# Kernel tuning notes

Hardware: AMD Instinct MI355X
Metric: run time of the kernel (lower is better)

The kernel has to match this reference:

```python
import jax, jax.numpy as jnp
import numpy as np

EPS = 1e-6
NH, NKV, HD = 16, 8, 256
WIN = 1024
NE, TOPK = 32, 4
H, I = 2816, 704


def _rmsnorm(x, w, eps=EPS):
    x32 = x.astype(jnp.float32)
    n = x32 * jax.lax.rsqrt(jnp.mean(x32 * x32, axis=-1, keepdims=True) + eps)
    return n.astype(x.dtype) * w


def _rotate_half(x):
    x1, x2 = jnp.split(x, 2, axis=-1)
    return jnp.concatenate([-x2, x1], axis=-1)


def setup_inputs() -> dict:
    B, S = 1, 512
    key = jax.random.key(0)
    ks = jax.random.split(key, 10)
    sc = 0.02
    hidden_states = jax.random.normal(ks[0], (B, S, H), jnp.float32)
    # rope tables (sliding_attention: theta=10000, full rotary over head_dim)
    pos = np.arange(S, dtype=np.float64)
    inv = 1.0 / (10000.0 ** (np.arange(0, HD, 2, dtype=np.float64) / HD))
    fr = pos[:, None] * inv[None, :]
    emb = np.concatenate([fr, fr], axis=-1)
    cos = jnp.asarray(np.cos(emb)[None], jnp.float32)
    sin = jnp.asarray(np.sin(emb)[None], jnp.float32)
    return dict(
        hidden_states=hidden_states, cos=cos, sin=sin,
        ln_in_w=jnp.ones((H,), jnp.float32),
        ln_post_attn_w=jnp.ones((H,), jnp.float32),
        ln_pre_ffn_w=jnp.ones((H,), jnp.float32),
        ln_post_ffn_w=jnp.ones((H,), jnp.float32),
        q_w=jax.random.normal(ks[1], (NH * HD, H), jnp.float32) * sc,
        k_w=jax.random.normal(ks[2], (NKV * HD, H), jnp.float32) * sc,
        v_w=jax.random.normal(ks[3], (NKV * HD, H), jnp.float32) * sc,
        o_w=jax.random.normal(ks[4], (H, NH * HD), jnp.float32) * sc,
        q_norm_w=jnp.ones((HD,), jnp.float32),
        k_norm_w=jnp.ones((HD,), jnp.float32),
        router_w=jax.random.normal(ks[5], (NE, H), jnp.float32) * sc,
        router_scale=jnp.ones((H,), jnp.float32),
        w_gate=jax.random.normal(ks[6], (NE, I, H), jnp.float32) * sc,
        w_up=jax.random.normal(ks[7], (NE, I, H), jnp.float32) * sc,
        w_down=jax.random.normal(ks[8], (NE, H, I), jnp.float32) * sc,
    )


def reference(hidden_states, cos, sin, ln_in_w, ln_post_attn_w, ln_pre_ffn_w,
              ln_post_ffn_w, q_w, k_w, v_w, o_w, q_norm_w, k_norm_w,
              router_w, router_scale, w_gate, w_up, w_down):
    B, S, _ = hidden_states.shape
    # ---- attention block ----
    res = hidden_states
    h = _rmsnorm(hidden_states, ln_in_w)
    q = (h @ q_w.T).reshape(B, S, NH, HD)
    k = (h @ k_w.T).reshape(B, S, NKV, HD)
    v = (h @ v_w.T).reshape(B, S, NKV, HD)
    q = _rmsnorm(q, q_norm_w)
    k = _rmsnorm(k, k_norm_w)
    v = _rmsnorm(v, jnp.float32(1.0))  # v_norm has no scale
    c, s = cos[:, :, None, :], sin[:, :, None, :]
    q = q * c + _rotate_half(q) * s
    k = k * c + _rotate_half(k) * s
    kr = jnp.repeat(k, NH // NKV, axis=2)  # GQA expand
    vr = jnp.repeat(v, NH // NKV, axis=2)
    scores = jnp.einsum('bqnd,bknd->bnqk', q, kr)  # softmax scale = 1.0
    ii = jnp.arange(S)[:, None]
    jj = jnp.arange(S)[None, :]
    mask = (jj <= ii) & ((ii - jj) < WIN)  # causal + sliding window
    scores = jnp.where(mask, scores, jnp.finfo(scores.dtype).min)
    attn = jax.nn.softmax(scores, axis=-1)
    o = jnp.einsum('bnqk,bknd->bqnd', attn, vr).reshape(B, S, NH * HD)
    h = _rmsnorm(o @ o_w.T, ln_post_attn_w)
    x = res + h
    # ---- MoE block ----
    res = x
    h = _rmsnorm(x, ln_pre_ffn_w)
    t = h.reshape(B * S, H)
    # router: RMSNorm(no scale) * hidden^-0.5 * scale -> linear -> softmax -> topk
    t32 = t.astype(jnp.float32)
    n = (t32 * jax.lax.rsqrt(jnp.mean(t32 * t32, -1, keepdims=True) + EPS)).astype(t.dtype)
    n = n * (H ** -0.5) * router_scale
    probs = jax.nn.softmax(n @ router_w.T, axis=-1)
    topw, topi = jax.lax.top_k(probs, TOPK)
    topw = topw / jnp.sum(topw, axis=-1, keepdims=True)
    T = t.shape[0]
    combine = jnp.zeros((T, NE), t.dtype).at[jnp.arange(T)[:, None], topi].add(topw)
    # gated MLP per expert (dense eval + sparse combine == torch_moe math)
    g = jnp.einsum('th,eih->eti', t, w_gate)
    u = jnp.einsum('th,eih->eti', t, w_up)
    a = jax.nn.gelu(g, approximate=True) * u
    y = jnp.einsum('eti,ehi->eth', a, w_down)  # [E,T,H]
    moe = jnp.einsum('te,eth->th', combine, y).reshape(B, S, H)
    moe = _rmsnorm(moe, ln_post_ffn_w)
    return res + moe
```

## Files before the change

### kernel.cpp

```cpp
#include <hip/hip_runtime.h>

static constexpr int T_S   = 512;
static constexpr int H_DIM = 2816;
static constexpr int HD_   = 256;
static constexpr int N_E   = 32;
static constexpr int TOPK_ = 4;
static constexpr int I_DIM = 704;
static constexpr int Q_N   = 4096;
static constexpr int KV_N  = 2048;
static constexpr int QKV_N = 8192;
static constexpr float EPS_ = 1e-6f;

typedef __attribute__((ext_vector_type(4))) float f32x4;
typedef __attribute__((ext_vector_type(8))) short bf16x8;

static __device__ __forceinline__ ushort f2bf(float f) {
  uint u = __float_as_uint(f);
  u += 0x7fffu + ((u >> 16) & 1u);
  return (ushort)(u >> 16);
}
static __device__ __forceinline__ float bf2f(ushort u) {
  return __uint_as_float((uint)u << 16);
}
static __device__ __forceinline__ void split2(float x, ushort& h, ushort& l2) {
  h = f2bf(x);
  l2 = f2bf(x - bf2f(h));
}
static __device__ __forceinline__ void split8(const float4& a, const float4& b,
                                              uint4& H, uint4& L) {
  ushort h0,l0,h1,l1,h2,l2,h3,l3,h4,l4,h5,l5,h6,l6,h7,l7;
  split2(a.x,h0,l0); split2(a.y,h1,l1); split2(a.z,h2,l2); split2(a.w,h3,l3);
  split2(b.x,h4,l4); split2(b.y,h5,l5); split2(b.z,h6,l6); split2(b.w,h7,l7);
  H = (uint4){ (uint)h0|((uint)h1<<16), (uint)h2|((uint)h3<<16),
               (uint)h4|((uint)h5<<16), (uint)h6|((uint)h7<<16) };
  L = (uint4){ (uint)l0|((uint)l1<<16), (uint)l2|((uint)l3<<16),
               (uint)l4|((uint)l5<<16), (uint)l6|((uint)l7<<16) };
}
static __device__ __forceinline__ uint4 pack8(const float4& a, const float4& b) {
  return (uint4){ (uint)f2bf(a.x)|((uint)f2bf(a.y)<<16), (uint)f2bf(a.z)|((uint)f2bf(a.w)<<16),
                  (uint)f2bf(b.x)|((uint)f2bf(b.y)<<16), (uint)f2bf(b.z)|((uint)f2bf(b.w)<<16) };
}

static __device__ __forceinline__ float wave_sum(float v) {
  #pragma unroll
  for (int off = 1; off < 64; off <<= 1) v += __shfl_xor(v, off);
  return v;
}
static __device__ __forceinline__ float block_sum256(float v, float* sm) {
  v = wave_sum(v);
  int w = threadIdx.x >> 6, l = threadIdx.x & 63;
  if (l == 0) sm[w] = v;
  __syncthreads();
  float r = sm[0] + sm[1] + sm[2] + sm[3];
  __syncthreads();
  return r;
}

__global__ __launch_bounds__(256) void k_ln_in(
    const float* __restrict__ hid, const float* __restrict__ w,
    ushort* __restrict__ hhi, ushort* __restrict__ hlo) {
  __shared__ float sm[4];
  int t = blockIdx.x, tid = threadIdx.x;
  const float* row = hid + (size_t)t * H_DIM;
  float x[11]; float s = 0.f;
  #pragma unroll
  for (int j = 0; j < 11; ++j) { x[j] = row[tid + j*256]; s += x[j]*x[j]; }
  s = block_sum256(s, sm);
  float r = rsqrtf(s / (float)H_DIM + EPS_);
  #pragma unroll
  for (int j = 0; j < 11; ++j) {
    int idx = tid + j*256;
    float val = x[j]*r*w[idx];
    ushort h, l2; split2(val, h, l2);
    hhi[(size_t)t*H_DIM + idx] = h;
    hlo[(size_t)t*H_DIM + idx] = l2;
  }
}

__global__ __launch_bounds__(256, 2) void k_gemm_qkv(
    const ushort* __restrict__ Ah, const ushort* __restrict__ Al,
    const float* __restrict__ qw, const float* __restrict__ kw,
    const float* __restrict__ vw, float* __restrict__ Cp) {
  const int K = H_DIM, KS = H_DIM/2, NSs = KS/32;
  __shared__ ushort Ash[4][129][8], Asl[4][129][8];
  __shared__ ushort Bsh[4][65][8],  Bsl[4][65][8];
  int tid = threadIdx.x, w = tid >> 6, l = tid & 63;
  int n0 = blockIdx.x * 64, m0 = blockIdx.y * 128, kz = blockIdx.z;
  int kbase = kz * KS;
  const float* Bp = (n0 < Q_N) ? qw + (size_t)n0*K
                  : (n0 < Q_N+KV_N) ? kw + (size_t)(n0-Q_N)*K
                  : vw + (size_t)(n0-Q_N-KV_N)*K;
  float* C = Cp + (size_t)kz * T_S * QKV_N;
  const int l15 = l & 15, lq = l >> 4;
  const int wm = w >> 1, wn = w & 1;
  const int sar = tid >> 2, sak = tid & 3;
  const ushort* aph = Ah + (size_t)(m0 + sar)*K + kbase + sak*8;
  const ushort* apl = Al + (size_t)(m0 + sar)*K + kbase + sak*8;
  const float*  bp  = Bp + (size_t)sar*K + kbase + sak*8;
  uint4 arh0 = *(const uint4*)(aph);
  uint4 arh1 = *(const uint4*)(aph + (size_t)64*K);
  uint4 arl0 = *(const uint4*)(apl);
  uint4 arl1 = *(const uint4*)(apl + (size_t)64*K);
  float4 brA = *(const float4*)(bp), brB = *(const float4*)(bp + 4);
  f32x4 acc[4][2];
  #pragma unroll
  for (int a = 0; a < 4; ++a)
    #pragma unroll
    for (int b = 0; b < 2; ++b) acc[a][b] = (f32x4){0.f,0.f,0.f,0.f};
  for (int t = 0; t < NSs; ++t) {
    *(uint4*)&Ash[sak][sar][0]    = arh0;
    *(uint4*)&Ash[sak][64+sar][0] = arh1;
    *(uint4*)&Asl[sak][sar][0]    = arl0;
    *(uint4*)&Asl[sak][64+sar][0] = arl1;
    { uint4 H, L; split8(brA, brB, H, L);
      *(uint4*)&Bsh[sak][sar][0] = H;
      *(uint4*)&Bsl[sak][sar][0] = L; }
    __syncthreads();
    if (t + 1 < NSs) {
      int k0 = (t+1)*32;
      arh0 = *(const uint4*)(aph + k0);
      arh1 = *(const uint4*)(aph + (size_t)64*K + k0);
      arl0 = *(const uint4*)(apl + k0);
      arl1 = *(const uint4*)(apl + (size_t)64*K + k0);
      brA = *(const float4*)(bp + k0); brB = *(const float4*)(bp + k0 + 4);
    }
    bf16x8 bh[2], bl[2];
    #pragma unroll
    for (int nf = 0; nf < 2; ++nf) {
      bh[nf] = *(bf16x8*)&Bsh[lq][wn*32 + nf*16 + l15][0];
      bl[nf] = *(bf16x8*)&Bsl[lq][wn*32 + nf*16 + l15][0];
    }
    #pragma unroll
    for (int mf = 0; mf < 4; ++mf) {
      bf16x8 ah = *(bf16x8*)&Ash[lq][wm*64 + mf*16 + l15][0];
      bf16x8 al = *(bf16x8*)&Asl[lq][wm*64 + mf*16 + l15][0];
      #pragma unroll
      for (int nf = 0; nf < 2; ++nf) {
        acc[mf][nf] = __builtin_amdgcn_mfma_f32_16x16x32_bf16(ah, bh[nf], acc[mf][nf], 0, 0, 0);
        acc[mf][nf] = __builtin_amdgcn_mfma_f32_16x16x32_bf16(ah, bl[nf], acc[mf][nf], 0, 0, 0);
        acc[mf][nf] = __builtin_amdgcn_mfma_f32_16x16x32_bf16(al, bh[nf], acc[mf][nf], 0, 0, 0);
      }
    }
    __syncthreads();
  }
  #pragma unroll
  for (int mf = 0; mf < 4; ++mf)
    #pragma unroll
    for (int nf = 0; nf < 2; ++nf)
      #pragma unroll
      for (int r = 0; r < 4; ++r)
        C[(size_t)(m0 + wm*64 + mf*16 + lq*4 + r)*QKV_N + n0 + wn*32 + nf*16 + l15] = acc[mf][nf][r];
}

__global__ __launch_bounds__(64) void k_norm_rope(
    const float* __restrict__ qkvf0, const float* __restrict__ qkvf1,
    const float* __restrict__ cosb, const float* __restrict__ sinb,
    const float* __restrict__ qnw, const float* __restrict__ knw,
    ushort* __restrict__ qh, ushort* __restrict__ ql,
    ushort* __restrict__ vth, ushort* __restrict__ vtl) {
  int bid = blockIdx.x;
  int token = bid >> 5, ch = bid & 31;
  int l = threadIdx.x;
  int col; const float* wp = nullptr; bool rope = true; int vch = -1;
// ... 196 lines not shown
  const ushort* apl = Al + (size_t)(m0 + sar)*K + kbase + sak*8;
  const float*  bp  = ow + (size_t)(n0 + sar)*K + kbase + sak*8;
  uint4 arh0 = *(const uint4*)(aph);
  uint4 arh1 = *(const uint4*)(aph + (size_t)64*K);
  uint4 arl0 = *(const uint4*)(apl);
  uint4 arl1 = *(const uint4*)(apl + (size_t)64*K);
  float4 brA = *(const float4*)(bp), brB = *(const float4*)(bp + 4);
  f32x4 acc[4][2];
  #pragma unroll
  for (int a = 0; a < 4; ++a)
    #pragma unroll
    for (int b = 0; b < 2; ++b) acc[a][b] = (f32x4){0.f,0.f,0.f,0.f};
  for (int t = 0; t < NSs; ++t) {
    *(uint4*)&Ash[sak][sar][0]    = arh0;
    *(uint4*)&Ash[sak][64+sar][0] = arh1;
    *(uint4*)&Asl[sak][sar][0]    = arl0;
    *(uint4*)&Asl[sak][64+sar][0] = arl1;
    { uint4 H, L; split8(brA, brB, H, L);
      *(uint4*)&Bsh[sak][sar][0] = H;
      *(uint4*)&Bsl[sak][sar][0] = L; }
    __syncthreads();
    if (t + 1 < NSs) {
      int k0 = (t+1)*32;
      arh0 = *(const uint4*)(aph + k0);
      arh1 = *(const uint4*)(aph + (size_t)64*K + k0);
      arl0 = *(const uint4*)(apl + k0);
      arl1 = *(const uint4*)(apl + (size_t)64*K + k0);
      brA = *(const float4*)(bp + k0); brB = *(const float4*)(bp + k0 + 4);
    }
    bf16x8 bh[2], bl[2];
    #pragma unroll
    for (int nf = 0; nf < 2; ++nf) {
      bh[nf] = *(bf16x8*)&Bsh[lq][wn*32 + nf*16 + l15][0];
      bl[nf] = *(bf16x8*)&Bsl[lq][wn*32 + nf*16 + l15][0];
    }
    #pragma unroll
    for (int mf = 0; mf < 4; ++mf) {
      bf16x8 ah = *(bf16x8*)&Ash[lq][wm*64 + mf*16 + l15][0];
      bf16x8 al = *(bf16x8*)&Asl[lq][wm*64 + mf*16 + l15][0];
      #pragma unroll
      for (int nf = 0; nf < 2; ++nf) {
        acc[mf][nf] = __builtin_amdgcn_mfma_f32_16x16x32_bf16(ah, bh[nf], acc[mf][nf], 0, 0, 0);
        acc[mf][nf] = __builtin_amdgcn_mfma_f32_16x16x32_bf16(ah, bl[nf], acc[mf][nf], 0, 0, 0);
        acc[mf][nf] = __builtin_amdgcn_mfma_f32_16x16x32_bf16(al, bh[nf], acc[mf][nf], 0, 0, 0);
      }
    }
    __syncthreads();
  }
  #pragma unroll
  for (int mf = 0; mf < 4; ++mf)
    #pragma unroll
    for (int nf = 0; nf < 2; ++nf)
      #pragma unroll
      for (int r = 0; r < 4; ++r)
        C[(size_t)(m0 + wm*64 + mf*16 + lq*4 + r)*H_DIM + n0 + wn*32 + nf*16 + l15] = acc[mf][nf][r];
}

__global__ void k_zero_counts(int* counts) {
  if (threadIdx.x < N_E) counts[threadIdx.x] = 0;
}

__global__ __launch_bounds__(256) void k_fuse_router(
    const float* __restrict__ hid, const float* __restrict__ aproj0,
    const float* __restrict__ aproj1,
    const float* __restrict__ w_pa, const float* __restrict__ w_pf,
    const float* __restrict__ rscale, const float* __restrict__ rw,
    float* __restrict__ xout, ushort* __restrict__ tbf,
    float* __restrict__ topw, int* __restrict__ counts, int* __restrict__ lists) {
  __shared__ float sm[4];
  __shared__ float nrow[H_DIM];
  __shared__ float lg[N_E];
  int t = blockIdx.x, tid = threadIdx.x;
  float ap[11], hd[11]; float s = 0.f;
  #pragma unroll
  for (int j = 0; j < 11; ++j) {
    int idx = tid + j*256;
    ap[j] = aproj0[(size_t)t*H_DIM + idx] + aproj1[(size_t)t*H_DIM + idx];
    hd[j] = hid[(size_t)t*H_DIM + idx];
    s += ap[j]*ap[j];
  }
  s = block_sum256(s, sm);
  float r1 = rsqrtf(s / (float)H_DIM + EPS_);
  float x[11]; float s2 = 0.f;
  #pragma unroll
  for (int j = 0; j < 11; ++j) {
    int idx = tid + j*256;
    x[j] = hd[j] + ap[j]*r1*w_pa[idx];
    s2 += x[j]*x[j];
    xout[(size_t)t*H_DIM + idx] = x[j];
  }
  s2 = block_sum256(s2, sm);
  float r2 = rsqrtf(s2 / (float)H_DIM + EPS_);
  float tv[11]; float s3 = 0.f;
  #pragma unroll
  for (int j = 0; j < 11; ++j) {
    int idx = tid + j*256;
    tv[j] = x[j]*r2*w_pf[idx];
    s3 += tv[j]*tv[j];
    tbf[(size_t)t*H_DIM + idx] = f2bf(tv[j]);
  }
  s3 = block_sum256(s3, sm);
  float r3 = rsqrtf(s3 / (float)H_DIM + EPS_) * rsqrtf((float)H_DIM);
  #pragma unroll
  for (int j = 0; j < 11; ++j) {
    int idx = tid + j*256;
    nrow[idx] = tv[j]*r3*rscale[idx];
  }
  __syncthreads();
  int w = tid >> 6, l = tid & 63;
  #pragma unroll
  for (int ei = 0; ei < 8; ++ei) {
    int e = w*8 + ei;
    const float* rwp = rw + (size_t)e*H_DIM;
    float p = 0.f;
    #pragma unroll 4
    for (int j = 0; j < 44; ++j) p += nrow[l + j*64] * rwp[l + j*64];
    p = wave_sum(p);
    if (l == 0) lg[e] = p;
  }
  __syncthreads();
  if (w == 0) {
    float le = (l < 32) ? lg[l] : -3e38f;
    float m = le;
    #pragma unroll
    for (int off = 1; off < 64; off <<= 1) m = fmaxf(m, __shfl_xor(m, off));
    float p = (l < 32) ? __expf(le - m) : -2.f;
    float v = p; int vi = (l < 32) ? l : 999;
    float selv[TOPK_]; int seli[TOPK_];
    for (int sx = 0; sx < TOPK_; ++sx) {
      float bv = v; int bi = vi;
      #pragma unroll
      for (int off = 1; off < 64; off <<= 1) {
        float ov = __shfl_xor(bv, off); int oi = __shfl_xor(bi, off);
        if (ov > bv || (ov == bv && oi < bi)) { bv = ov; bi = oi; }
      }
      selv[sx] = bv; seli[sx] = bi;
      if (vi == bi) v = -1.f;
    }
    if (l == 0) {
      float wsum = selv[0]+selv[1]+selv[2]+selv[3];
      for (int sx = 0; sx < TOPK_; ++sx) {
        topw[t*TOPK_ + sx] = selv[sx]/wsum;
        int e = seli[sx];
        int pos = atomicAdd(&counts[e], 1);
        lists[e*T_S + pos] = t*TOPK_ + sx;
      }
    }
  }
}

__global__ __launch_bounds__(256, 2) void k_moe_gateup(
    const ushort* __restrict__ tbf, const float* __restrict__ wg,
    const float* __restrict__ wu, const int* __restrict__ counts,
    const int* __restrict__ lists, ushort* __restrict__ abf) {
  const int K = H_DIM, NS = K/32;
  __shared__ ushort As[4][65][8];
  __shared__ ushort Bg[4][129][8], Bu[4][129][8];
  __shared__ int lls[64];
  int tid = threadIdx.x, w = tid >> 6, l = tid & 63;
  int e = blockIdx.y, n0 = blockIdx.x * 128, m0 = blockIdx.z * 64;
  int ne = counts[e];
  if (m0 >= ne) return;
  const int* list = lists + e*T_S;
  if (tid < 64) lls[tid] = (m0 + tid < ne) ? list[m0 + tid] : list[0];
  __syncthreads();
  const int l15 = l & 15, lq = l >> 4;
  const int sar = tid >> 2, sak = tid & 3;
  int tok = lls[sar] >> 2;
  const ushort* ap = tbf + (size_t)tok*K + sak*8;
  int ng0 = n0 + sar, ng1 = n0 + 64 + sar;
  ng0 = (ng0 < I_DIM) ? ng0 : I_DIM-1;
  ng1 = (ng1 < I_DIM) ? ng1 : I_DIM-1;
  const float* gp0 = wg + ((size_t)e*I_DIM + ng0)*K + sak*8;
  const float* gp1 = wg + ((size_t)e*I_DIM + ng1)*K + sak*8;
  const float* up0 = wu + ((size_t)e*I_DIM + ng0)*K + sak*8;
  const float* up1 = wu + ((size_t)e*I_DIM + ng1)*K + sak*8;
  uint4 ar; float4 g0a,g0b,g1a,g1b,u0a,u0b,u1a,u1b;
  ar  = *(const uint4*)(ap);
  g0a = *(const float4*)(gp0); g0b = *(const float4*)(gp0 + 4);
  g1a = *(const float4*)(gp1); g1b = *(const float4*)(gp1 + 4);
  u0a = *(const float4*)(up0); u0b = *(const float4*)(up0 + 4);
  u1a = *(const float4*)(up1); u1b = *(const float4*)(up1 + 4);
  f32x4 ag[4][2], au[4][2];
  #pragma unroll
  for (int a = 0; a < 4; ++a)
    #pragma unroll
    for (int b = 0; b < 2; ++b) { ag[a][b] = (f32x4){0.f,0.f,0.f,0.f}; au[a][b] = (f32x4){0.f,0.f,0.f,0.f}; }
  for (int t = 0; t < NS; ++t) {
    *(uint4*)&As[sak][sar][0] = ar;
    *(uint4*)&Bg[sak][sar][0]    = pack8(g0a, g0b);
    *(uint4*)&Bg[sak][64+sar][0] = pack8(g1a, g1b);
    *(uint4*)&Bu[sak][sar][0]    = pack8(u0a, u0b);
    *(uint4*)&Bu[sak][64+sar][0] = pack8(u1a, u1b);
    __syncthreads();
    if (t + 1 < NS) {
      int k0 = (t+1)*32;
      ar  = *(const uint4*)(ap + k0);
      g0a = *(const float4*)(gp0 + k0); g0b = *(const float4*)(gp0 + k0 + 4);
      g1a = *(const float4*)(gp1 + k0); g1b = *(const float4*)(gp1 + k0 + 4);
      u0a = *(const float4*)(up0 + k0); u0b = *(const float4*)(up0 + k0 + 4);
      u1a = *(const float4*)(up1 + k0); u1b = *(const float4*)(up1 + k0 + 4);
    }
    bf16x8 bg[2], bu[2];
    #pragma unroll
    for (int nf = 0; nf < 2; ++nf) {
      bg[nf] = *(bf16x8*)&Bg[lq][w*32 + nf*16 + l15][0];
      bu[nf] = *(bf16x8*)&Bu[lq][w*32 + nf*16 + l15][0];
    }
    #pragma unroll
    for (int mf = 0; mf < 4; ++mf) {
      bf16x8 af = *(bf16x8*)&As[lq][mf*16 + l15][0];
      #pragma unroll
      for (int nf = 0; nf < 2; ++nf) {
        ag[mf][nf] = __builtin_amdgcn_mfma_f32_16x16x32_bf16(af, bg[nf], ag[mf][nf], 0, 0, 0);
        au[mf][nf] = __builtin_amdgcn_mfma_f32_16x16x32_bf16(af, bu[nf], au[mf][nf], 0, 0, 0);
      }
    }
    __syncthreads();
  }
  #pragma unroll
  for (int mf = 0; mf < 4; ++mf) {
    #pragma unroll
    for (int r = 0; r < 4; ++r) {
      int row = mf*16 + lq*4 + r;
      if (m0 + row < ne) {
        #pragma unroll
        for (int nf = 0; nf < 2; ++nf) {
          int col = n0 + w*32 + nf*16 + l15;
          if (col < I_DIM) {
            float g = ag[mf][nf][r], u = au[mf][nf][r];
            float th = tanhf(0.7978845608f*(g + 0.044715f*g*g*g));
            float a = 0.5f*g*(1.f + th)*u;
            abf[((size_t)e*T_S + m0 + row)*I_DIM + col] = f2bf(a);
          }
        }
      }
    }
  }
}

__global__ __launch_bounds__(256, 2) void k_moe_down(
    const ushort* __restrict__ abf, const float* __restrict__ wd,
    const int* __restrict__ counts, const int* __restrict__ lists,
    float* __restrict__ yall) {
  const int K = I_DIM, NS = K/32;
  __shared__ ushort As[4][65][8];
  __shared__ ushort Bs[4][129][8];
  __shared__ int lls[64];
  int tid = threadIdx.x, w = tid >> 6, l = tid & 63;
  int e = blockIdx.y, n0 = blockIdx.x * 128, m0 = blockIdx.z * 64;
  int ne = counts[e];
  if (m0 >= ne) return;
  const int* list = lists + e*T_S;
  if (tid < 64) lls[tid] = (m0 + tid < ne) ? list[m0 + tid] : 0;
  __syncthreads();
  const int l15 = l & 15, lq = l >> 4;
  const int sar = tid >> 2, sak = tid & 3;
  const ushort* ap = abf + ((size_t)e*T_S + m0 + sar)*K + sak*8;
  const float* bp0 = wd + ((size_t)e*H_DIM + n0 + sar)*K + sak*8;
  const float* bp1 = wd + ((size_t)e*H_DIM + n0 + 64 + sar)*K + sak*8;
  uint4 ar; float4 b0a,b0b,b1a,b1b;
  ar  = *(const uint4*)(ap);
  b0a = *(const float4*)(bp0); b0b = *(const float4*)(bp0 + 4);
  b1a = *(const float4*)(bp1); b1b = *(const float4*)(bp1 + 4);
  f32x4 acc[4][2];
  #pragma unroll
  for (int a = 0; a < 4; ++a)
    #pragma unroll
    for (int b = 0; b < 2; ++b) acc[a][b] = (f32x4){0.f,0.f,0.f,0.f};
  for (int t = 0; t < NS; ++t) {
    *(uint4*)&As[sak][sar][0] = ar;
    *(uint4*)&Bs[sak][sar][0]    = pack8(b0a, b0b);
    *(uint4*)&Bs[sak][64+sar][0] = pack8(b1a, b1b);
    __syncthreads();
    if (t + 1 < NS) {
      int k0 = (t+1)*32;
      ar  = *(const uint4*)(ap + k0);
      b0a = *(const float4*)(bp0 + k0); b0b = *(const float4*)(bp0 + k0 + 4);
      b1a = *(const float4*)(bp1 + k0); b1b = *(const float4*)(bp1 + k0 + 4);
    }
    bf16x8 bf[2];
    #pragma unroll
    for (int nf = 0; nf < 2; ++nf)
      bf[nf] = *(bf16x8*)&Bs[lq][w*32 + nf*16 + l15][0];
    #pragma unroll
    for (int mf = 0; mf < 4; ++mf) {
      bf16x8 af = *(bf16x8*)&As[lq][mf*16 + l15][0];
      #pragma unroll
      for (int nf = 0; nf < 2; ++nf)
        acc[mf][nf] = __builtin_amdgcn_mfma_f32_16x16x32_bf16(af, bf[nf], acc[mf][nf], 0, 0, 0);
    }
    __syncthreads();
  }
  #pragma unroll
  for (int mf = 0; mf < 4; ++mf)
    #pragma unroll
    for (int r = 0; r < 4; ++r) {
      int row = mf*16 + lq*4 + r;
      if (m0 + row < ne) {
        int en = lls[row];
        #pragma unroll
        for (int nf = 0; nf < 2; ++nf)
          yall[(size_t)en*H_DIM + n0 + w*32 + nf*16 + l15] = acc[mf][nf][r];
      }
    }
}

__global__ __launch_bounds__(256) void k_combine(
    const float* __restrict__ yall, const float* __restrict__ topw,
    const float* __restrict__ xin, const float* __restrict__ w_pff,
    float* __restrict__ out) {
  __shared__ float sm[4];
  int t = blockIdx.x, tid = threadIdx.x;
  float w0 = topw[t*4+0], w1 = topw[t*4+1], w2 = topw[t*4+2], w3 = topw[t*4+3];
  const float* y0 = yall + (size_t)(t*4+0)*H_DIM;
  const float* y1 = yall + (size_t)(t*4+1)*H_DIM;
  const float* y2 = yall + (size_t)(t*4+2)*H_DIM;
  const float* y3 = yall + (size_t)(t*4+3)*H_DIM;
  float m[11]; float s = 0.f;
  #pragma unroll
  for (int j = 0; j < 11; ++j) {
    int idx = tid + j*256;
    m[j] = w0*y0[idx] + w1*y1[idx] + w2*y2[idx] + w3*y3[idx];
    s += m[j]*m[j];
  }
  s = block_sum256(s, sm);
  float r = rsqrtf(s / (float)H_DIM + EPS_);
  #pragma unroll
  for (int j = 0; j < 11; ++j) {
    int idx = tid + j*256;
    out[(size_t)t*H_DIM + idx] = xin[(size_t)t*H_DIM + idx] + m[j]*r*w_pff[idx];
  }
}

extern "C" void kernel_launch(void* const* d_in, const int* in_sizes, int n_in,
                              void* d_out, int out_size, void* d_ws, size_t ws_size,
                              hipStream_t stream) {
  (void)in_sizes; (void)n_in; (void)out_size; (void)ws_size;
  const float* hid   = (const float*)d_in[0];
  const float* cosb  = (const float*)d_in[1];
  const float* sinb  = (const float*)d_in[2];
  const float* w_in  = (const float*)d_in[3];
  const float* w_pa  = (const float*)d_in[4];
  const float* w_pf  = (const float*)d_in[5];
  const float* w_pff = (const float*)d_in[6];
  const float* qw    = (const float*)d_in[7];
  const float* kw    = (const float*)d_in[8];
  const float* vw    = (const float*)d_in[9];
  const float* ow    = (const float*)d_in[10];
  const float* qnw   = (const float*)d_in[11];
  const float* knw   = (const float*)d_in[12];
  const float* rw    = (const float*)d_in[13];
  const float* rsc   = (const float*)d_in[14];
  const float* wg    = (const float*)d_in[15];
  const float* wu    = (const float*)d_in[16];
  const float* wd    = (const float*)d_in[17];

  char* ws = (char*)d_ws;
  size_t off = 0;
  auto alloc = [&](size_t sz) { size_t o = off; off += (sz + 255) & ~(size_t)255; return o; };
  size_t oR1  = alloc(33554432);
  size_t ohh  = alloc((size_t)T_S*H_DIM*2);
  size_t ohl  = alloc((size_t)T_S*H_DIM*2);
  size_t oqh  = alloc((size_t)T_S*QKV_N*2);
  size_t oql  = alloc((size_t)T_S*QKV_N*2);
  size_t ovh  = alloc((size_t)8*HD_*T_S*2);
  size_t ovl  = alloc((size_t)8*HD_*T_S*2);
  size_t ox   = alloc((size_t)T_S*H_DIM*4);
  size_t otbf = alloc((size_t)T_S*H_DIM*2);
  size_t otw  = alloc((size_t)T_S*TOPK_*4);
  size_t ocnt = alloc((size_t)N_E*4);
  size_t olst = alloc((size_t)N_E*T_S*4);

  const size_t APRJ_SLICE = (size_t)T_S * H_DIM * 4;

  float*  qkvf0 = (float*)(ws + oR1);
  float*  qkvf1 = (float*)(ws + oR1 + 16777216);
  ushort* o_hi  = (ushort*)(ws + oR1);
  ushort* o_lo  = (ushort*)(ws + oR1 + 4194304);
  float*  aprj0 = (float*)(ws + oR1 + 8388608);
  float*  aprj1 = (float*)(ws + oR1 + 8388608 + APRJ_SLICE);
  float*  yall  = (float*)(ws + oR1);
  ushort* abf   = (ushort*)(ws + ohh);

  k_ln_in<<<dim3(T_S), dim3(256), 0, stream>>>(hid, w_in, (ushort*)(ws+ohh), (ushort*)(ws+ohl));
  k_gemm_qkv<<<dim3(128, 4, 2), dim3(256), 0, stream>>>((ushort*)(ws+ohh), (ushort*)(ws+ohl),
                                                        qw, kw, vw, qkvf0);
  k_norm_rope<<<dim3(T_S*32), dim3(64), 0, stream>>>(qkvf0, qkvf1, cosb, sinb, qnw, knw,
                                                     (ushort*)(ws+oqh), (ushort*)(ws+oql),
                                                     (ushort*)(ws+ovh), (ushort*)(ws+ovl));
  k_attn<<<dim3(8, 16), dim3(256), 0, stream>>>((ushort*)(ws+oqh), (ushort*)(ws+oql),
                                                (ushort*)(ws+ovh), (ushort*)(ws+ovl), o_hi, o_lo);
  k_gemm_oproj<<<dim3(44, 4, 2), dim3(256), 0, stream>>>(o_hi, o_lo, ow, aprj0);
  k_zero_counts<<<dim3(1), dim3(64), 0, stream>>>((int*)(ws+ocnt));
  k_fuse_router<<<dim3(T_S), dim3(256), 0, stream>>>(hid, aprj0, aprj1, w_pa, w_pf, rsc, rw,
                                                     (float*)(ws+ox), (ushort*)(ws+otbf),
                                                     (float*)(ws+otw), (int*)(ws+ocnt), (int*)(ws+olst));
  k_moe_gateup<<<dim3(6, N_E, 8), dim3(256), 0, stream>>>((ushort*)(ws+otbf), wg, wu,
                                                          (int*)(ws+ocnt), (int*)(ws+olst), abf);
  k_moe_down<<<dim3(22, N_E, 8), dim3(256), 0, stream>>>(abf, wd,
                                                         (int*)(ws+ocnt), (int*)(ws+olst), yall);
  k_combine<<<dim3(T_S), dim3(256), 0, stream>>>(yall, (float*)(ws+otw), (float*)(ws+ox),
                                                 w_pff, (float*)d_out);
}
```

Measured before the change: 623.1 us.

## Retile MoE gate/up to narrow N tiles and deepen K step to 64

The gate/up expert GEMM tile shrinks from 128 to 32 output columns, so the grid grows from 6 to 22 column blocks per expert. With 704 = 22*32 the ragged-edge clamping goes away, and the four waves are arranged 2x2 over M and N. Both the gate/up and down kernels now stage 64 K-elements per iteration instead of 32, halving the number of barrier-separated steps and issuing wider per-thread global loads. The cost is that the token activations are reloaded by more blocks, with fewer MFMAs per wave per step and more LDS and registers in use.

Result: slower. 684.5 us (+9.9%).

```diff
diff --git a/kernel.cpp b/kernel.cpp
--- a/kernel.cpp
+++ b/kernel.cpp
@@ -512,99 +512,82 @@
     const ushort* __restrict__ tbf, const float* __restrict__ wg,
     const float* __restrict__ wu, const int* __restrict__ counts,
     const int* __restrict__ lists, ushort* __restrict__ abf) {
-  const int K = H_DIM, NS = K/32;
-  __shared__ ushort As[4][65][8];
-  __shared__ ushort Bg[4][129][8], Bu[4][129][8];
+  const int K = H_DIM, NS = K/64;
+  __shared__ ushort As[8][65][8];
+  __shared__ ushort Bg[8][33][8], Bu[8][33][8];
   __shared__ int lls[64];
   int tid = threadIdx.x, w = tid >> 6, l = tid & 63;
-  int e = blockIdx.y, n0 = blockIdx.x * 128, m0 = blockIdx.z * 64;
+  int e = blockIdx.y, n0 = blockIdx.x * 32, m0 = blockIdx.z * 64;
   int ne = counts[e];
   if (m0 >= ne) return;
   const int* list = lists + e*T_S;
   if (tid < 64) lls[tid] = (m0 + tid < ne) ? list[m0 + tid] : list[0];
   __syncthreads();
   const int l15 = l & 15, lq = l >> 4;
-  const int sar = tid >> 2, sak = tid & 3;
-  int tok = lls[sar] >> 2;
-  const ushort* ap = tbf + (size_t)tok*K + sak*8;
-  int ng0 = n0 + sar, ng1 = n0 + 64 + sar;
-  ng0 = (ng0 < I_DIM) ? ng0 : I_DIM-1;
-  ng1 = (ng1 < I_DIM) ? ng1 : I_DIM-1;
-  const float* gp0 = wg + ((size_t)e*I_DIM + ng0)*K + sak*8;
-  const float* gp1 = wg + ((size_t)e*I_DIM + ng1)*K + sak*8;
-  const float* up0 = wu + ((size_t)e*I_DIM + ng0)*K + sak*8;
-  const float* up1 = wu + ((size_t)e*I_DIM + ng1)*K + sak*8;
-  uint4 ar; float4 g0a,g0b,g1a,g1b,u0a,u0b,u1a,u1b;
-  ar  = *(const uint4*)(ap);
-  g0a = *(const float4*)(gp0); g0b = *(const float4*)(gp0 + 4);
-  g1a = *(const float4*)(gp1); g1b = *(const float4*)(gp1 + 4);
-  u0a = *(const float4*)(up0); u0b = *(const float4*)(up0 + 4);
-  u1a = *(const float4*)(up1); u1b = *(const float4*)(up1 + 4);
-  f32x4 ag[4][2], au[4][2];
-  #pragma unroll
-  for (int a = 0; a < 4; ++a)
-    #pragma unroll
-    for (int b = 0; b < 2; ++b) { ag[a][b] = (f32x4){0.f,0.f,0.f,0.f}; au[a][b] = (f32x4){0.f,0.f,0.f,0.f}; }
+  const int arow = tid >> 2, aop = (tid & 3) * 2;
+  int tok = lls[arow] >> 2;
+  const ushort* ap = tbf + (size_t)tok*K + aop*8;
+  const int bhalf = tid >> 7, brow = (tid & 127) >> 2, bq = tid & 3;
+  const float* bptr = (bhalf ? wu : wg) + ((size_t)e*I_DIM + n0 + brow)*K + bq*16;
+  uint4 a0 = *(const uint4*)(ap), a1 = *(const uint4*)(ap + 8);
+  float4 b0 = *(const float4*)(bptr),      b1 = *(const float4*)(bptr + 4);
+  float4 b2 = *(const float4*)(bptr + 8),  b3 = *(const float4*)(bptr + 12);
+  const int wm = w >> 1, wn = w & 1;
+  f32x4 ag[2], au[2];
+  #pragma unroll
+  for (int i = 0; i < 2; ++i) { ag[i] = (f32x4){0.f,0.f,0.f,0.f}; au[i] = (f32x4){0.f,0.f,0.f,0.f}; }
   for (int t = 0; t < NS; ++t) {
-    *(uint4*)&As[sak][sar][0] = ar;
-    *(uint4*)&Bg[sak][sar][0]    = pack8(g0a, g0b);
-    *(uint4*)&Bg[sak][64+sar][0] = pack8(g1a, g1b);
-    *(uint4*)&Bu[sak][sar][0]    = pack8(u0a, u0b);
-    *(uint4*)&Bu[sak][64+sar][0] = pack8(u1a, u1b);
+    *(uint4*)&As[aop][arow][0]   = a0;
+    *(uint4*)&As[aop+1][arow][0] = a1;
+    if (bhalf == 0) {
+      *(uint4*)&Bg[bq*2][brow][0]   = pack8(b0, b1);
+      *(uint4*)&Bg[bq*2+1][brow][0] = pack8(b2, b3);
+    } else {
+      *(uint4*)&Bu[bq*2][brow][0]   = pack8(b0, b1);
+      *(uint4*)&Bu[bq*2+1][brow][0] = pack8(b2, b3);
+    }
     __syncthreads();
     if (t + 1 < NS) {
-      int k0 = (t+1)*32;
-      ar  = *(const uint4*)(ap + k0);
-      g0a = *(const float4*)(gp0 + k0); g0b = *(const float4*)(gp0 + k0 + 4);
-      g1a = *(const float4*)(gp1 + k0); g1b = *(const float4*)(gp1 + k0 + 4);
-      u0a = *(const float4*)(up0 + k0); u0b = *(const float4*)(up0 + k0 + 4);
-      u1a = *(const float4*)(up1 + k0); u1b = *(const float4*)(up1 + k0 + 4);
-    }
-    bf16x8 bg[2], bu[2];
-    #pragma unroll
-    for (int nf = 0; nf < 2; ++nf) {
-      bg[nf] = *(bf16x8*)&Bg[lq][w*32 + nf*16 + l15][0];
-      bu[nf] = *(bf16x8*)&Bu[lq][w*32 + nf*16 + l15][0];
-    }
-    #pragma unroll
-    for (int mf = 0; mf < 4; ++mf) {
-      bf16x8 af = *(bf16x8*)&As[lq][mf*16 + l15][0];
-      #pragma unroll
-      for (int nf = 0; nf < 2; ++nf) {
-        ag[mf][nf] = __builtin_amdgcn_mfma_f32_16x16x32_bf16(af, bg[nf], ag[mf][nf], 0, 0, 0);
-        au[mf][nf] = __builtin_amdgcn_mfma_f32_16x16x32_bf16(af, bu[nf], au[mf][nf], 0, 0, 0);
-      }
-    }
-    __syncthreads();
-  }
-  #pragma unroll
-  for (int mf = 0; mf < 4; ++mf) {
+      int k0 = (t+1)*64;
+      a0 = *(const uint4*)(ap + k0); a1 = *(const uint4*)(ap + k0 + 8);
+      b0 = *(const float4*)(bptr + k0);      b1 = *(const float4*)(bptr + k0 + 4);
+      b2 = *(const float4*)(bptr + k0 + 8);  b3 = *(const float4*)(bptr + k0 + 12);
+    }
+    #pragma unroll
+    for (int kc = 0; kc < 2; ++kc) {
+      int pl = kc*4 + lq;
+      bf16x8 bgf = *(bf16x8*)&Bg[pl][wn*16 + l15][0];
+      bf16x8 buf = *(bf16x8*)&Bu[pl][wn*16 + l15][0];
+      #pragma unroll
+      for (int mf = 0; mf < 2; ++mf) {
+        bf16x8 af = *(bf16x8*)&As[pl][wm*32 + mf*16 + l15][0];
+        ag[mf] = __builtin_amdgcn_mfma_f32_16x16x32_bf16(af, bgf, ag[mf], 0, 0, 0);
+        au[mf] = __builtin_amdgcn_mfma_f32_16x16x32_bf16(af, buf, au[mf], 0, 0, 0);
+      }
+    }
+    __syncthreads();
+  }
+  #pragma unroll
+  for (int mf = 0; mf < 2; ++mf)
     #pragma unroll
     for (int r = 0; r < 4; ++r) {
-      int row = mf*16 + lq*4 + r;
+      int row = wm*32 + mf*16 + lq*4 + r;
       if (m0 + row < ne) {
-        #pragma unroll
-        for (int nf = 0; nf < 2; ++nf) {
-          int col = n0 + w*32 + nf*16 + l15;
-          if (col < I_DIM) {
-            float g = ag[mf][nf][r], u = au[mf][nf][r];
-            float th = tanhf(0.7978845608f*(g + 0.044715f*g*g*g));
-            float a = 0.5f*g*(1.f + th)*u;
-            abf[((size_t)e*T_S + m0 + row)*I_DIM + col] = f2bf(a);
-          }
-        }
-      }
-    }
-  }
+        float g = ag[mf][r], u = au[mf][r];
+        float th = tanhf(0.7978845608f*(g + 0.044715f*g*g*g));
+        float a = 0.5f*g*(1.f + th)*u;
+        abf[((size_t)e*T_S + m0 + row)*I_DIM + n0 + wn*16 + l15] = f2bf(a);
+      }
+    }
 }
 
 __global__ __launch_bounds__(256, 2) void k_moe_down(
     const ushort* __restrict__ abf, const float* __restrict__ wd,
     const int* __restrict__ counts, const int* __restrict__ lists,
     float* __restrict__ yall) {
-  const int K = I_DIM, NS = K/32;
-  __shared__ ushort As[4][65][8];
-  __shared__ ushort Bs[4][129][8];
+  const int K = I_DIM, NS = K/64;
+  __shared__ ushort As[8][65][8];
+  __shared__ ushort Bs[8][129][8];
   __shared__ int lls[64];
   int tid = threadIdx.x, w = tid >> 6, l = tid & 63;
   int e = blockIdx.y, n0 = blockIdx.x * 128, m0 = blockIdx.z * 64;
@@ -614,40 +597,47 @@
   if (tid < 64) lls[tid] = (m0 + tid < ne) ? list[m0 + tid] : 0;
   __syncthreads();
   const int l15 = l & 15, lq = l >> 4;
-  const int sar = tid >> 2, sak = tid & 3;
-  const ushort* ap = abf + ((size_t)e*T_S + m0 + sar)*K + sak*8;
-  const float* bp0 = wd + ((size_t)e*H_DIM + n0 + sar)*K + sak*8;
-  const float* bp1 = wd + ((size_t)e*H_DIM + n0 + 64 + sar)*K + sak*8;
-  uint4 ar; float4 b0a,b0b,b1a,b1b;
-  ar  = *(const uint4*)(ap);
-  b0a = *(const float4*)(bp0); b0b = *(const float4*)(bp0 + 4);
-  b1a = *(const float4*)(bp1); b1b = *(const float4*)(bp1 + 4);
+  const int arow = tid >> 2, aop = (tid & 3) * 2;
+  const ushort* ap = abf + ((size_t)e*T_S + m0 + arow)*K + aop*8;
+  const int brow = tid >> 1, bo = (tid & 1) * 4;
+  const float* bp = wd + ((size_t)e*H_DIM + n0 + brow)*K + bo*8;
+  uint4 a0 = *(const uint4*)(ap), a1 = *(const uint4*)(ap + 8);
+  float4 c0 = *(const float4*)(bp),      c1 = *(const float4*)(bp + 4);
+  float4 c2 = *(const float4*)(bp + 8),  c3 = *(const float4*)(bp + 12);
+  float4 c4 = *(const float4*)(bp + 16), c5 = *(const float4*)(bp + 20);
+  float4 c6 = *(const float4*)(bp + 24), c7 = *(const float4*)(bp + 28);
   f32x4 acc[4][2];
   #pragma unroll
   for (int a = 0; a < 4; ++a)
     #pragma unroll
     for (int b = 0; b < 2; ++b) acc[a][b] = (f32x4){0.f,0.f,0.f,0.f};
   for (int t = 0; t < NS; ++t) {
-    *(uint4*)&As[sak][sar][0] = ar;
-    *(uint4*)&Bs[sak][sar][0]    = pack8(b0a, b0b);
-    *(uint4*)&Bs[sak][64+sar][0] = pack8(b1a, b1b);
+    *(uint4*)&As[aop][arow][0]   = a0;
+    *(uint4*)&As[aop+1][arow][0] = a1;
+    *(uint4*)&Bs[bo][brow][0]   = pack8(c0, c1);
+    *(uint4*)&Bs[bo+1][brow][0] = pack8(c2, c3);
+    *(uint4*)&Bs[bo+2][brow][0] = pack8(c4, c5);
+    *(uint4*)&Bs[bo+3][brow][0] = pack8(c6, c7);
     __syncthreads();
     if (t + 1 < NS) {
-      int k0 = (t+1)*32;
-      ar  = *(const uint4*)(ap + k0);
-      b0a = *(const float4*)(bp0 + k0); b0b = *(const float4*)(bp0 + k0 + 4);
-      b1a = *(const float4*)(bp1 + k0); b1b = *(const float4*)(bp1 + k0 + 4);
-    }
-    bf16x8 bf[2];
-    #pragma unroll
-    for (int nf = 0; nf < 2; ++nf)
-      bf[nf] = *(bf16x8*)&Bs[lq][w*32 + nf*16 + l15][0];
-    #pragma unroll
-    for (int mf = 0; mf < 4; ++mf) {
-      bf16x8 af = *(bf16x8*)&As[lq][mf*16 + l15][0];
-      #pragma unroll
-      for (int nf = 0; nf < 2; ++nf)
-        acc[mf][nf] = __builtin_amdgcn_mfma_f32_16x16x32_bf16(af, bf[nf], acc[mf][nf], 0, 0, 0);
+      int k0 = (t+1)*64;
+      a0 = *(const uint4*)(ap + k0); a1 = *(const uint4*)(ap + k0 + 8);
+      c0 = *(const float4*)(bp + k0);      c1 = *(const float4*)(bp + k0 + 4);
+      c2 = *(const float4*)(bp + k0 + 8);  c3 = *(const float4*)(bp + k0 + 12);
+      c4 = *(const float4*)(bp + k0 + 16); c5 = *(const float4*)(bp + k0 + 20);
+      c6 = *(const float4*)(bp + k0 + 24); c7 = *(const float4*)(bp + k0 + 28);
+    }
+    #pragma unroll
+    for (int kc = 0; kc < 2; ++kc) {
+      int pl = kc*4 + lq;
+      bf16x8 bf0 = *(bf16x8*)&Bs[pl][w*32 + l15][0];
+      bf16x8 bf1 = *(bf16x8*)&Bs[pl][w*32 + 16 + l15][0];
+      #pragma unroll
+      for (int mf = 0; mf < 4; ++mf) {
+        bf16x8 af = *(bf16x8*)&As[pl][mf*16 + l15][0];
+        acc[mf][0] = __builtin_amdgcn_mfma_f32_16x16x32_bf16(af, bf0, acc[mf][0], 0, 0, 0);
+        acc[mf][1] = __builtin_amdgcn_mfma_f32_16x16x32_bf16(af, bf1, acc[mf][1], 0, 0, 0);
+      }
     }
     __syncthreads();
   }
@@ -755,8 +745,8 @@
   k_fuse_router<<<dim3(T_S), dim3(256), 0, stream>>>(hid, aprj0, aprj1, w_pa, w_pf, rsc, rw,
                                                      (float*)(ws+ox), (ushort*)(ws+otbf),
                                                      (float*)(ws+otw), (int*)(ws+ocnt), (int*)(ws+olst));
-  k_moe_gateup<<<dim3(6, N_E, 8), dim3(256), 0, stream>>>((ushort*)(ws+otbf), wg, wu,
-                                                          (int*)(ws+ocnt), (int*)(ws+olst), abf);
+  k_moe_gateup<<<dim3(22, N_E, 8), dim3(256), 0, stream>>>((ushort*)(ws+otbf), wg, wu,
+                                                           (int*)(ws+ocnt), (int*)(ws+olst), abf);
   k_moe_down<<<dim3(22, N_E, 8), dim3(256), 0, stream>>>(abf, wd,
                                                          (int*)(ws+ocnt), (int*)(ws+olst), yall);
   k_combine<<<dim3(T_S), dim3(256), 0, stream>>>(yall, (float*)(ws+otw), (float*)(ws+ox),
```

## Split-K MoE GEMMs with 128-row tiles and separate GELU reduction pass

Applied to the files above, without the earlier changes.

The gate/up GEMM is split four ways along K with 128x64 tiles, writing fp32 partials indexed by slot. A new kernel sums the partials and applies GELU*up into bf16. The down GEMM is split two ways along K with 128x128 tiles, and the combine kernel adds the two partials. The aim is to fill the GPU better despite the uneven per-expert token counts and to reuse weight loads across more rows. The cost is extra fp32 partial traffic, a larger workspace and one more kernel launch.

New measurement: 610.9 us. No clear change (-1.9%).

```diff
diff --git a/kernel.cpp b/kernel.cpp
--- a/kernel.cpp
+++ b/kernel.cpp
@@ -9,6 +9,7 @@
 static constexpr int Q_N   = 4096;
 static constexpr int KV_N  = 2048;
 static constexpr int QKV_N = 8192;
+static constexpr int NSLOT = 2048;
 static constexpr float EPS_ = 1e-6f;
 
 typedef __attribute__((ext_vector_type(4))) float f32x4;
@@ -511,176 +512,200 @@
 __global__ __launch_bounds__(256, 2) void k_moe_gateup(
     const ushort* __restrict__ tbf, const float* __restrict__ wg,
     const float* __restrict__ wu, const int* __restrict__ counts,
-    const int* __restrict__ lists, ushort* __restrict__ abf) {
-  const int K = H_DIM, NS = K/32;
-  __shared__ ushort As[4][65][8];
-  __shared__ ushort Bg[4][129][8], Bu[4][129][8];
-  __shared__ int lls[64];
+    const int* __restrict__ lists, float* __restrict__ pg, float* __restrict__ pu) {
+  const int K = H_DIM, KS = K/4, NS = KS/32;
+  __shared__ ushort As[4][129][8];
+  __shared__ ushort Bg[4][65][8], Bu[4][65][8];
+  __shared__ int lls[128];
   int tid = threadIdx.x, w = tid >> 6, l = tid & 63;
-  int e = blockIdx.y, n0 = blockIdx.x * 128, m0 = blockIdx.z * 64;
+  int e = blockIdx.y, n0 = blockIdx.x * 64;
+  int mz = blockIdx.z >> 2, kz = blockIdx.z & 3;
+  int m0 = mz * 128, kbase = kz * KS;
   int ne = counts[e];
   if (m0 >= ne) return;
   const int* list = lists + e*T_S;
-  if (tid < 64) lls[tid] = (m0 + tid < ne) ? list[m0 + tid] : list[0];
+  if (tid < 128) lls[tid] = (m0 + tid < ne) ? list[m0 + tid] : list[0];
   __syncthreads();
   const int l15 = l & 15, lq = l >> 4;
-  const int sar = tid >> 2, sak = tid & 3;
-  int tok = lls[sar] >> 2;
-  const ushort* ap = tbf + (size_t)tok*K + sak*8;
-  int ng0 = n0 + sar, ng1 = n0 + 64 + sar;
-  ng0 = (ng0 < I_DIM) ? ng0 : I_DIM-1;
-  ng1 = (ng1 < I_DIM) ? ng1 : I_DIM-1;
-  const float* gp0 = wg + ((size_t)e*I_DIM + ng0)*K + sak*8;
-  const float* gp1 = wg + ((size_t)e*I_DIM + ng1)*K + sak*8;
-  const float* up0 = wu + ((size_t)e*I_DIM + ng0)*K + sak*8;
-  const float* up1 = wu + ((size_t)e*I_DIM + ng1)*K + sak*8;
-  uint4 ar; float4 g0a,g0b,g1a,g1b,u0a,u0b,u1a,u1b;
-  ar  = *(const uint4*)(ap);
-  g0a = *(const float4*)(gp0); g0b = *(const float4*)(gp0 + 4);
-  g1a = *(const float4*)(gp1); g1b = *(const float4*)(gp1 + 4);
-  u0a = *(const float4*)(up0); u0b = *(const float4*)(up0 + 4);
-  u1a = *(const float4*)(up1); u1b = *(const float4*)(up1 + 4);
+  const int wm = w >> 1, wn = w & 1;
+  const int arow = tid >> 1, aoct = (tid & 1) * 2;
+  const ushort* ap = tbf + (size_t)(lls[arow] >> 2)*K + kbase + aoct*8;
+  const int bhalf = tid >> 7, brow = (tid & 127) >> 1, boct = (tid & 1) * 2;
+  const float* bp = (bhalf ? wu : wg) + ((size_t)e*I_DIM + n0 + brow)*K + kbase + boct*8;
+  uint4 a0 = *(const uint4*)(ap), a1 = *(const uint4*)(ap + 8);
+  float4 b0 = *(const float4*)(bp),     b1 = *(const float4*)(bp + 4);
+  float4 b2 = *(const float4*)(bp + 8), b3 = *(const float4*)(bp + 12);
   f32x4 ag[4][2], au[4][2];
   #pragma unroll
   for (int a = 0; a < 4; ++a)
     #pragma unroll
     for (int b = 0; b < 2; ++b) { ag[a][b] = (f32x4){0.f,0.f,0.f,0.f}; au[a][b] = (f32x4){0.f,0.f,0.f,0.f}; }
   for (int t = 0; t < NS; ++t) {
-    *(uint4*)&As[sak][sar][0] = ar;
-    *(uint4*)&Bg[sak][sar][0]    = pack8(g0a, g0b);
-    *(uint4*)&Bg[sak][64+sar][0] = pack8(g1a, g1b);
-    *(uint4*)&Bu[sak][sar][0]    = pack8(u0a, u0b);
-    *(uint4*)&Bu[sak][64+sar][0] = pack8(u1a, u1b);
+    *(uint4*)&As[aoct][arow][0]   = a0;
+    *(uint4*)&As[aoct+1][arow][0] = a1;
+    if (bhalf == 0) {
+      *(uint4*)&Bg[boct][brow][0]   = pack8(b0, b1);
+      *(uint4*)&Bg[boct+1][brow][0] = pack8(b2, b3);
+    } else {
+      *(uint4*)&Bu[boct][brow][0]   = pack8(b0, b1);
+      *(uint4*)&Bu[boct+1][brow][0] = pack8(b2, b3);
+    }
     __syncthreads();
     if (t + 1 < NS) {
       int k0 = (t+1)*32;
-      ar  = *(const uint4*)(ap + k0);
-      g0a = *(const float4*)(gp0 + k0); g0b = *(const float4*)(gp0 + k0 + 4);
-      g1a = *(const float4*)(gp1 + k0); g1b = *(const float4*)(gp1 + k0 + 4);
-      u0a = *(const float4*)(up0 + k0); u0b = *(const float4*)(up0 + k0 + 4);
-      u1a = *(const float4*)(up1 + k0); u1b = *(const float4*)(up1 + k0 + 4);
-    }
-    bf16x8 bg[2], bu[2];
+      a0 = *(const uint4*)(ap + k0); a1 = *(const uint4*)(ap + k0 + 8);
+      b0 = *(const float4*)(bp + k0);     b1 = *(const float4*)(bp + k0 + 4);
+      b2 = *(const float4*)(bp + k0 + 8); b3 = *(const float4*)(bp + k0 + 12);
+    }
+    bf16x8 bgf[2], buf_[2];
     #pragma unroll
     for (int nf = 0; nf < 2; ++nf) {
-      bg[nf] = *(bf16x8*)&Bg[lq][w*32 + nf*16 + l15][0];
-      bu[nf] = *(bf16x8*)&Bu[lq][w*32 + nf*16 + l15][0];
+      bgf[nf]  = *(bf16x8*)&Bg[lq][wn*32 + nf*16 + l15][0];
+      buf_[nf] = *(bf16x8*)&Bu[lq][wn*32 + nf*16 + l15][0];
     }
     #pragma unroll
     for (int mf = 0; mf < 4; ++mf) {
-      bf16x8 af = *(bf16x8*)&As[lq][mf*16 + l15][0];
+      bf16x8 af = *(bf16x8*)&As[lq][wm*64 + mf*16 + l15][0];
       #pragma unroll
       for (int nf = 0; nf < 2; ++nf) {
-        ag[mf][nf] = __builtin_amdgcn_mfma_f32_16x16x32_bf16(af, bg[nf], ag[mf][nf], 0, 0, 0);
-        au[mf][nf] = __builtin_amdgcn_mfma_f32_16x16x32_bf16(af, bu[nf], au[mf][nf], 0, 0, 0);
-      }
-    }
-    __syncthreads();
-  }
-  #pragma unroll
-  for (int mf = 0; mf < 4; ++mf) {
+        ag[mf][nf] = __builtin_amdgcn_mfma_f32_16x16x32_bf16(af, bgf[nf],  ag[mf][nf], 0, 0, 0);
+        au[mf][nf] = __builtin_amdgcn_mfma_f32_16x16x32_bf16(af, buf_[nf], au[mf][nf], 0, 0, 0);
+      }
+    }
+    __syncthreads();
+  }
+  const size_t PSL = (size_t)NSLOT * I_DIM;
+  #pragma unroll
+  for (int mf = 0; mf < 4; ++mf)
     #pragma unroll
     for (int r = 0; r < 4; ++r) {
-      int row = mf*16 + lq*4 + r;
+      int row = wm*64 + mf*16 + lq*4 + r;
       if (m0 + row < ne) {
+        size_t base = (size_t)kz*PSL + (size_t)lls[row]*I_DIM + n0 + wn*32;
         #pragma unroll
         for (int nf = 0; nf < 2; ++nf) {
-          int col = n0 + w*32 + nf*16 + l15;
-          if (col < I_DIM) {
-            float g = ag[mf][nf][r], u = au[mf][nf][r];
-            float th = tanhf(0.7978845608f*(g + 0.044715f*g*g*g));
-            float a = 0.5f*g*(1.f + th)*u;
-            abf[((size_t)e*T_S + m0 + row)*I_DIM + col] = f2bf(a);
-          }
+          pg[base + nf*16 + l15] = ag[mf][nf][r];
+          pu[base + nf*16 + l15] = au[mf][nf][r];
         }
       }
     }
-  }
+}
+
+__global__ __launch_bounds__(192) void k_gelu_reduce(
+    const float* __restrict__ pg, const float* __restrict__ pu,
+    ushort* __restrict__ abf) {
+  int sidx = blockIdx.x, c = threadIdx.x;
+  if (c >= 176) return;
+  const size_t S4 = (size_t)NSLOT * I_DIM / 4;
+  const float4* g = (const float4*)(pg + (size_t)sidx*I_DIM) + c;
+  const float4* u = (const float4*)(pu + (size_t)sidx*I_DIM) + c;
+  float4 gs = g[0], us = u[0];
+  #pragma unroll
+  for (int k = 1; k < 4; ++k) {
+    float4 gk = g[k*S4], uk = u[k*S4];
+    gs.x += gk.x; gs.y += gk.y; gs.z += gk.z; gs.w += gk.w;
+    us.x += uk.x; us.y += uk.y; us.z += uk.z; us.w += uk.w;
+  }
+  float go[4] = {gs.x, gs.y, gs.z, gs.w}, uo[4] = {us.x, us.y, us.z, us.w};
+  ushort o[4];
+  #pragma unroll
+  for (int i = 0; i < 4; ++i) {
+    float gg = go[i];
+    float th = tanhf(0.7978845608f*(gg + 0.044715f*gg*gg*gg));
+    o[i] = f2bf(0.5f*gg*(1.f + th)*uo[i]);
+  }
+  *(ushort4*)(abf + (size_t)sidx*I_DIM + c*4) = *(ushort4*)o;
 }
 
 __global__ __launch_bounds__(256, 2) void k_moe_down(
     const ushort* __restrict__ abf, const float* __restrict__ wd,
     const int* __restrict__ counts, const int* __restrict__ lists,
-    float* __restrict__ yall) {
-  const int K = I_DIM, NS = K/32;
-  __shared__ ushort As[4][65][8];
+    float* __restrict__ yp) {
+  const int K = I_DIM, KS = K/2, NS = KS/32;
+  __shared__ ushort As[4][129][8];
   __shared__ ushort Bs[4][129][8];
-  __shared__ int lls[64];
+  __shared__ int lls[128];
   int tid = threadIdx.x, w = tid >> 6, l = tid & 63;
-  int e = blockIdx.y, n0 = blockIdx.x * 128, m0 = blockIdx.z * 64;
+  int e = blockIdx.y, n0 = blockIdx.x * 128;
+  int mz = blockIdx.z >> 1, kz = blockIdx.z & 1;
+  int m0 = mz * 128, kbase = kz * KS;
   int ne = counts[e];
   if (m0 >= ne) return;
   const int* list = lists + e*T_S;
-  if (tid < 64) lls[tid] = (m0 + tid < ne) ? list[m0 + tid] : 0;
+  if (tid < 128) lls[tid] = (m0 + tid < ne) ? list[m0 + tid] : 0;
   __syncthreads();
   const int l15 = l & 15, lq = l >> 4;
-  const int sar = tid >> 2, sak = tid & 3;
-  const ushort* ap = abf + ((size_t)e*T_S + m0 + sar)*K + sak*8;
-  const float* bp0 = wd + ((size_t)e*H_DIM + n0 + sar)*K + sak*8;
-  const float* bp1 = wd + ((size_t)e*H_DIM + n0 + 64 + sar)*K + sak*8;
-  uint4 ar; float4 b0a,b0b,b1a,b1b;
-  ar  = *(const uint4*)(ap);
-  b0a = *(const float4*)(bp0); b0b = *(const float4*)(bp0 + 4);
-  b1a = *(const float4*)(bp1); b1b = *(const float4*)(bp1 + 4);
-  f32x4 acc[4][2];
+  const int wm = w >> 1, wn = w & 1;
+  const int arow = tid >> 1, aoct = (tid & 1) * 2;
+  const ushort* ap = abf + (size_t)lls[arow]*K + kbase + aoct*8;
+  const int brow = tid >> 1, boct = (tid & 1) * 2;
+  const float* bp = wd + ((size_t)e*H_DIM + n0 + brow)*K + kbase + boct*8;
+  uint4 a0 = *(const uint4*)(ap), a1 = *(const uint4*)(ap + 8);
+  float4 b0 = *(const float4*)(bp),     b1 = *(const float4*)(bp + 4);
+  float4 b2 = *(const float4*)(bp + 8), b3 = *(const float4*)(bp + 12);
+  f32x4 acc[4][4];
   #pragma unroll
   for (int a = 0; a < 4; ++a)
     #pragma unroll
-    for (int b = 0; b < 2; ++b) acc[a][b] = (f32x4){0.f,0.f,0.f,0.f};
+    for (int b = 0; b < 4; ++b) acc[a][b] = (f32x4){0.f,0.f,0.f,0.f};
   for (int t = 0; t < NS; ++t) {
-    *(uint4*)&As[sak][sar][0] = ar;
-    *(uint4*)&Bs[sak][sar][0]    = pack8(b0a, b0b);
-    *(uint4*)&Bs[sak][64+sar][0] = pack8(b1a, b1b);
+    *(uint4*)&As[aoct][arow][0]   = a0;
+    *(uint4*)&As[aoct+1][arow][0] = a1;
+    *(uint4*)&Bs[boct][brow][0]   = pack8(b0, b1);
+    *(uint4*)&Bs[boct+1][brow][0] = pack8(b2, b3);
     __syncthreads();
     if (t + 1 < NS) {
       int k0 = (t+1)*32;
-      ar  = *(const uint4*)(ap + k0);
-      b0a = *(const float4*)(bp0 + k0); b0b = *(const float4*)(bp0 + k0 + 4);
-      b1a = *(const float4*)(bp1 + k0); b1b = *(const float4*)(bp1 + k0 + 4);
-    }
-    bf16x8 bf[2];
-    #pragma unroll
-    for (int nf = 0; nf < 2; ++nf)
-      bf[nf] = *(bf16x8*)&Bs[lq][w*32 + nf*16 + l15][0];
+      a0 = *(const uint4*)(ap + k0); a1 = *(const uint4*)(ap + k0 + 8);
+      b0 = *(const float4*)(bp + k0);     b1 = *(const float4*)(bp + k0 + 4);
+      b2 = *(const float4*)(bp + k0 + 8); b3 = *(const float4*)(bp + k0 + 12);
+    }
+    bf16x8 bf[4];
+    #pragma unroll
+    for (int nf = 0; nf < 4; ++nf)
+      bf[nf] = *(bf16x8*)&Bs[lq][wn*64 + nf*16 + l15][0];
     #pragma unroll
     for (int mf = 0; mf < 4; ++mf) {
-      bf16x8 af = *(bf16x8*)&As[lq][mf*16 + l15][0];
-      #pragma unroll
-      for (int nf = 0; nf < 2; ++nf)
+      bf16x8 af = *(bf16x8*)&As[lq][wm*64 + mf*16 + l15][0];
+      #pragma unroll
+      for (int nf = 0; nf < 4; ++nf)
         acc[mf][nf] = __builtin_amdgcn_mfma_f32_16x16x32_bf16(af, bf[nf], acc[mf][nf], 0, 0, 0);
     }
     __syncthreads();
   }
+  const size_t YSL = (size_t)NSLOT * H_DIM;
   #pragma unroll
   for (int mf = 0; mf < 4; ++mf)
     #pragma unroll
     for (int r = 0; r < 4; ++r) {
-      int row = mf*16 + lq*4 + r;
+      int row = wm*64 + mf*16 + lq*4 + r;
       if (m0 + row < ne) {
-        int en = lls[row];
+        size_t base = (size_t)kz*YSL + (size_t)lls[row]*H_DIM + n0 + wn*64;
         #pragma unroll
-        for (int nf = 0; nf < 2; ++nf)
-          yall[(size_t)en*H_DIM + n0 + w*32 + nf*16 + l15] = acc[mf][nf][r];
+        for (int nf = 0; nf < 4; ++nf)
+          yp[base + nf*16 + l15] = acc[mf][nf][r];
       }
     }
 }
 
 __global__ __launch_bounds__(256) void k_combine(
-    const float* __restrict__ yall, const float* __restrict__ topw,
+    const float* __restrict__ yp, const float* __restrict__ topw,
     const float* __restrict__ xin, const float* __restrict__ w_pff,
     float* __restrict__ out) {
   __shared__ float sm[4];
+  const size_t YSL = (size_t)NSLOT * H_DIM;
   int t = blockIdx.x, tid = threadIdx.x;
   float w0 = topw[t*4+0], w1 = topw[t*4+1], w2 = topw[t*4+2], w3 = topw[t*4+3];
-  const float* y0 = yall + (size_t)(t*4+0)*H_DIM;
-  const float* y1 = yall + (size_t)(t*4+1)*H_DIM;
-  const float* y2 = yall + (size_t)(t*4+2)*H_DIM;
-  const float* y3 = yall + (size_t)(t*4+3)*H_DIM;
+  const float* y0 = yp + (size_t)(t*4+0)*H_DIM;
+  const float* y1 = yp + (size_t)(t*4+1)*H_DIM;
+  const float* y2 = yp + (size_t)(t*4+2)*H_DIM;
+  const float* y3 = yp + (size_t)(t*4+3)*H_DIM;
   float m[11]; float s = 0.f;
   #pragma unroll
   for (int j = 0; j < 11; ++j) {
     int idx = tid + j*256;
-    m[j] = w0*y0[idx] + w1*y1[idx] + w2*y2[idx] + w3*y3[idx];
+    m[j] = w0*(y0[idx]+y0[YSL+idx]) + w1*(y1[idx]+y1[YSL+idx])
+         + w2*(y2[idx]+y2[YSL+idx]) + w3*(y3[idx]+y3[YSL+idx]);
     s += m[j]*m[j];
   }
   s = block_sum256(s, sm);
@@ -718,7 +743,7 @@
   char* ws = (char*)d_ws;
   size_t off = 0;
   auto alloc = [&](size_t sz) { size_t o = off; off += (sz + 255) & ~(size_t)255; return o; };
-  size_t oR1  = alloc(33554432);
+  size_t oR1  = alloc(46137344);
   size_t ohh  = alloc((size_t)T_S*H_DIM*2);
   size_t ohl  = alloc((size_t)T_S*H_DIM*2);
   size_t oqh  = alloc((size_t)T_S*QKV_N*2);
@@ -739,7 +764,9 @@
   ushort* o_lo  = (ushort*)(ws + oR1 + 4194304);
   float*  aprj0 = (float*)(ws + oR1 + 8388608);
   float*  aprj1 = (float*)(ws + oR1 + 8388608 + APRJ_SLICE);
-  float*  yall  = (float*)(ws + oR1);
+  float*  pg    = (float*)(ws + oR1);
+  float*  pu    = (float*)(ws + oR1 + 23068672);
+  float*  yp    = (float*)(ws + oR1);
   ushort* abf   = (ushort*)(ws + ohh);
 
   k_ln_in<<<dim3(T_S), dim3(256), 0, stream>>>(hid, w_in, (ushort*)(ws+ohh), (ushort*)(ws+ohl));
@@ -755,10 +782,11 @@
   k_fuse_router<<<dim3(T_S), dim3(256), 0, stream>>>(hid, aprj0, aprj1, w_pa, w_pf, rsc, rw,
                                                      (float*)(ws+ox), (ushort*)(ws+otbf),
                                                      (float*)(ws+otw), (int*)(ws+ocnt), (int*)(ws+olst));
-  k_moe_gateup<<<dim3(6, N_E, 8), dim3(256), 0, stream>>>((ushort*)(ws+otbf), wg, wu,
-                                                          (int*)(ws+ocnt), (int*)(ws+olst), abf);
+  k_moe_gateup<<<dim3(11, N_E, 16), dim3(256), 0, stream>>>((ushort*)(ws+otbf), wg, wu,
+                                                            (int*)(ws+ocnt), (int*)(ws+olst), pg, pu);
+  k_gelu_reduce<<<dim3(NSLOT), dim3(192), 0, stream>>>(pg, pu, abf);
   k_moe_down<<<dim3(22, N_E, 8), dim3(256), 0, stream>>>(abf, wd,
-                                                         (int*)(ws+ocnt), (int*)(ws+olst), yall);
-  k_combine<<<dim3(T_S), dim3(256), 0, stream>>>(yall, (float*)(ws+otw), (float*)(ws+ox),
+                                                         (int*)(ws+ocnt), (int*)(ws+olst), yp);
+  k_combine<<<dim3(T_S), dim3(256), 0, stream>>>(yp, (float*)(ws+otw), (float*)(ws+ox),
                                                  w_pff, (float*)d_out);
 }
```
